# Performance work log

Hardware: AMD Instinct MI355X
Metric: run time of the kernel (lower is better)

## Reference

```python
import jax, jax.numpy as jnp
from jax import lax
import numpy as np

B, DIM, H, W = 4, 256, 64, 64
C2 = 2 * DIM          # 512 internal channels
CB = DIM              # 256 channels per branch
NH = 8                # heads per branch (num_heads*2 // 2)
HD = CB // NH         # 32 head dim
SPLIT = 8
SCALE = HD ** -0.5
EPS = 1e-5


def layernorm(x, g, b):
    mu = jnp.mean(x, axis=-1, keepdims=True)
    var = jnp.mean(jnp.square(x - mu), axis=-1, keepdims=True)
    return (x - mu) * lax.rsqrt(var + EPS) * g + b


def lepe_branch(q, k, v, cw, cb, H_sp, W_sp):
    # q,k,v: [B, L, CB]; cross-shaped stripe-window attention with LePE
    nH, nW = H // H_sp, W // W_sp
    win = H_sp * W_sp

    def to_win(t):
        t = t.reshape(B, nH, H_sp, nW, W_sp, CB).transpose(0, 1, 3, 2, 4, 5)
        return t.reshape(B * nH * nW, win, NH, HD).transpose(0, 2, 1, 3)

    qw = to_win(q) * SCALE
    kw = to_win(k)
    # v as per-window images for depthwise LePE conv: [B*nH*nW, CB, H_sp, W_sp]
    v_img = v.reshape(B, nH, H_sp, nW, W_sp, CB).transpose(0, 1, 3, 5, 2, 4)
    v_img = v_img.reshape(B * nH * nW, CB, H_sp, W_sp)
    lepe = lax.conv_general_dilated(v_img, cw, (1, 1), 'SAME',
                                    feature_group_count=CB,
                                    dimension_numbers=('NCHW', 'OIHW', 'NCHW'))
    lepe = lepe + cb[None, :, None, None]
    vw = v_img.reshape(-1, NH, HD, win).transpose(0, 1, 3, 2)
    lepew = lepe.reshape(-1, NH, HD, win).transpose(0, 1, 3, 2)

    attn = jax.nn.softmax(jnp.einsum('bhid,bhjd->bhij', qw, kw), axis=-1)
    o = jnp.einsum('bhij,bhjd->bhid', attn, vw) + lepew
    # windows back to image token order: [B, H*W, CB]
    o = o.transpose(0, 2, 1, 3).reshape(B, nH, nW, H_sp, W_sp, CB)
    o = o.transpose(0, 1, 3, 2, 4, 5).reshape(B, H * W, CB)
    return o


def setup_inputs() -> dict:
    key = jax.random.key(0)
    ks = jax.random.split(key, 12)
    s = 0.02
    return {
        'x': jax.random.normal(ks[0], (B, DIM, H, W), jnp.float32),
        'w_embed': jax.random.normal(ks[1], (DIM, C2), jnp.float32) * s,
        'g1': 1.0 + jax.random.normal(ks[2], (C2,), jnp.float32) * s,
        'b1': jax.random.normal(ks[3], (C2,), jnp.float32) * s,
        'w_qkv': jax.random.normal(ks[4], (C2, 3 * C2), jnp.float32) * s,
        'conv_w0': jax.random.normal(ks[5], (CB, 1, 3, 3), jnp.float32) * s,
        'conv_b0': jax.random.normal(ks[6], (CB,), jnp.float32) * s,
        'conv_w1': jax.random.normal(ks[7], (CB, 1, 3, 3), jnp.float32) * s,
        'conv_b1': jax.random.normal(ks[8], (CB,), jnp.float32) * s,
        'w_proj': jax.random.normal(ks[9], (C2, C2), jnp.float32) * s,
        'b_proj': jax.random.normal(ks[10], (C2,), jnp.float32) * s,
        'w_out': jax.random.normal(ks[11], (C2, DIM), jnp.float32) * s,
    }


def reference(x, w_embed, g1, b1, w_qkv, conv_w0, conv_b0, conv_w1, conv_b1,
              w_proj, b_proj, w_out):
    L = H * W
    # b c h w -> b (h w) c, then embed to 2*dim
    xt = x.reshape(B, DIM, L).transpose(0, 2, 1)
    x2 = xt @ w_embed                          # [B, L, 512]
    img = layernorm(x2, g1, b1)
    qkv = (img @ w_qkv).reshape(B, L, 3, C2).transpose(2, 0, 1, 3)  # [3,B,L,512]
    q, k, v = qkv[0], qkv[1], qkv[2]
    # branch 0: horizontal stripes (H_sp=H, W_sp=split); branch 1: transpose
    o0 = lepe_branch(q[..., :CB], k[..., :CB], v[..., :CB], conv_w0, conv_b0, H, SPLIT)
    o1 = lepe_branch(q[..., CB:], k[..., CB:], v[..., CB:], conv_w1, conv_b1, SPLIT, W)
    att = jnp.concatenate([o0, o1], axis=2) @ w_proj + b_proj
    xo = x2 + att
    out = (xo @ w_out).transpose(0, 2, 1).reshape(B, DIM, H, W)
    vout = (v @ w_out).transpose(0, 2, 1).reshape(B, DIM, H, W)
    return out, vout
```

## Files before the change

kernel.cpp:

```cpp
#include <hip/hip_runtime.h>
#include <cstdint>

#define Bn 4
#define DIMn 256
#define Ln 4096
#define C2n 512
#define CBn 256
#define HDn 32
#define Mtot (Bn * Ln)

using bf16x8 = __attribute__((ext_vector_type(8))) short;
using f32x4 = __attribute__((ext_vector_type(4))) float;

static constexpr float kScale = 0.17677669529663687f;
static constexpr float kEps = 1e-5f;
static constexpr float kExpC = 0.17677669529663687f * 1.4426950408889634f;

__device__ __forceinline__ ushort f2bf(float f) {
  union {
    float f;
    unsigned u;
  } v;
  v.f = f;
  unsigned r = v.u + 0x7FFFu + ((v.u >> 16) & 1u);
  return (ushort)(r >> 16);
}

__device__ __forceinline__ float bf2f(ushort u) {
  union {
    unsigned u;
    float f;
  } v;
  v.u = (unsigned)u << 16;
  return v.f;
}

__device__ __forceinline__ unsigned cvtpk(float lo, float hi) {
  unsigned r;
  asm("v_cvt_pk_bf16_f32 %0, %1, %2" : "=v"(r) : "v"(lo), "v"(hi));
  return r;
}

__device__ __forceinline__ void gload16(const void* g, void* l) {
  __builtin_amdgcn_global_load_lds(
      (const __attribute__((address_space(1))) unsigned*)g,
      (__attribute__((address_space(3))) unsigned*)l, 16, 0, 0);
}

enum { G_EMBED = 0, G_QKV = 1, G_PROJ = 2, G_OUTT = 3 };

template <int MODE, int ND, int KD, int LDB>
__global__ __launch_bounds__(256) void gemm_bf(
    const ushort* __restrict__ A, const ushort* __restrict__ Bt,
    float* __restrict__ C, const ushort* __restrict__ resid,
    const float* __restrict__ bias, ushort* __restrict__ aux,
    size_t outBase) {
  constexpr int NT = ND / 128;
  __shared__ ushort As[128 * 64];
  __shared__ ushort Bs[128 * 64];

  const int tid = threadIdx.x;
  const int wid = tid >> 6;
  const int lane = tid & 63;
  const int m0 = (blockIdx.x / NT) * 128;
  const int n0 = (blockIdx.x % NT) * 128;

  const int gs = (wid < 2) ? KD : LDB;
  const ushort* gsrc = (wid < 2)
                           ? A + (size_t)(m0 + (wid & 1) * 64) * KD
                           : Bt + (size_t)(n0 + (wid & 1) * 64) * LDB;
  ushort* lbase = (wid < 2 ? As : Bs) + (wid & 1) * (64 * 64);
  const int r8 = lane >> 3;
  const int c8 = lane & 7;

  f32x4 acc[4][4];
#pragma unroll
  for (int i = 0; i < 4; ++i)
#pragma unroll
    for (int j = 0; j < 4; ++j) acc[i][j] = (f32x4){0.f, 0.f, 0.f, 0.f};

  const int wm = (wid & 1) * 64;
  const int wn = (wid >> 1) * 64;
  const int lr = lane & 15;
  const int kq = lane >> 4;

  for (int k0 = 0; k0 < KD; k0 += 64) {
    __syncthreads();
#pragma unroll
    for (int i = 0; i < 8; ++i) {
      const ushort* g = gsrc + (size_t)(i * 8 + r8) * gs + (k0 + c8 * 8);
      gload16(g, lbase + i * 512);
    }
    __syncthreads();
#pragma unroll
    for (int kk = 0; kk < 2; ++kk) {
      bf16x8 af[4], bfr[4];
#pragma unroll
      for (int i = 0; i < 4; ++i)
        af[i] = *(const bf16x8*)(As + (wm + i * 16 + lr) * 64 +
                                 (kk * 4 + kq) * 8);
#pragma unroll
      for (int j = 0; j < 4; ++j)
        bfr[j] = *(const bf16x8*)(Bs + (wn + j * 16 + lr) * 64 +
                                  (kk * 4 + kq) * 8);
#pragma unroll
      for (int i = 0; i < 4; ++i)
#pragma unroll
        for (int j = 0; j < 4; ++j)
          acc[i][j] = __builtin_amdgcn_mfma_f32_16x16x32_bf16(
              af[i], bfr[j], acc[i][j], 0, 0, 0);
    }
  }

#pragma unroll
  for (int i = 0; i < 4; ++i) {
#pragma unroll
    for (int j = 0; j < 4; ++j) {
#pragma unroll
      for (int t = 0; t < 4; ++t) {
        const int mr = m0 + wm + i * 16 + kq * 4 + t;
        const int nc = n0 + wn + j * 16 + lr;
        float val = acc[i][j][t];
        if constexpr (MODE == G_EMBED) {
          aux[(size_t)mr * 512 + nc] = f2bf(val);
        } else if constexpr (MODE == G_QKV) {
          if (nc < 512) val *= kExpC;
          aux[(size_t)mr * 1536 + nc] = f2bf(val);
        } else if constexpr (MODE == G_PROJ) {
          const float v2 =
              val + bf2f(resid[(size_t)mr * 512 + nc]) + bias[nc];
          aux[(size_t)mr * 512 + nc] = f2bf(v2);
        } else {
          C[outBase + ((size_t)(nc >> 12)) * ((size_t)DIMn * Ln) +
            (size_t)mr * Ln + (nc & 4095)] = val;
        }
      }
    }
  }
}

__global__ __launch_bounds__(256) void cvt_w(const float* __restrict__ in,
                                             ushort* __restrict__ out,
                                             int lgK, int N) {
  const int t = blockIdx.x * 256 + threadIdx.x;
  const int K = 1 << lgK;
  const int n = t >> lgK;
  const int k = t & (K - 1);
  out[t] = f2bf(in[(size_t)k * N + n]);
}

__global__ __launch_bounds__(256) void cvt_x(const float* __restrict__ x,
                                             ushort* __restrict__ xe) {
  __shared__ ushort tile[64][65];
  const int blk = blockIdx.x;
  const int lt = blk & 63;
  const int ct = (blk >> 6) & 3;
  const int b = blk >> 8;
  const int l0 = lt * 64, c0 = ct * 64;
  const int t = threadIdx.x;
  const int lanel = t & 63;
  const int grp = t >> 6;
#pragma unroll
  for (int it = 0; it < 16; ++it) {
    const int c = grp * 16 + it;
    tile[c][lanel] =
        f2bf(x[(size_t)b * (DIMn * Ln) + (size_t)(c0 + c) * Ln + l0 + lanel]);
  }
  __syncthreads();
#pragma unroll
  for (int it = 0; it < 16; ++it) {
    const int l = grp * 16 + it;
    xe[((size_t)b * Ln + l0 + l) * 256 + c0 + lanel] = tile[lanel][l];
  }
}

__global__ __launch_bounds__(128) void ln_fuse(const ushort* __restrict__ x2,
                                               const float* __restrict__ g1,
                                               const float* __restrict__ b1,
                                               ushort* __restrict__ xln) {
  const int row = blockIdx.x;
  const int t = threadIdx.x;
  const ushort4 u4 = *(const ushort4*)&x2[(size_t)row * 512 + t * 4];
  float v[4] = {bf2f(u4.x), bf2f(u4.y), bf2f(u4.z), bf2f(u4.w)};
  float s = v[0] + v[1] + v[2] + v[3];
  float s2 = v[0] * v[0] + v[1] * v[1] + v[2] * v[2] + v[3] * v[3];
#pragma unroll
  for (int off = 32; off > 0; off >>= 1) {
    s += __shfl_down(s, off);
    s2 += __shfl_down(s2, off);
  }
  __shared__ float red[4];
  if ((t & 63) == 0) {
    red[t >> 6] = s;
    red[2 + (t >> 6)] = s2;
  }
  __syncthreads();
  const float S = red[0] + red[1];
  const float S2 = red[2] + red[3];
  const float mu = S * (1.f / 512.f);
  const float rs = rsqrtf(S2 * (1.f / 512.f) - mu * mu + kEps);
  const float4 g = *(const float4*)&g1[t * 4];
  const float4 bb = *(const float4*)&b1[t * 4];
  ushort4 o;
  o.x = f2bf((v[0] - mu) * rs * g.x + bb.x);
  o.y = f2bf((v[1] - mu) * rs * g.y + bb.y);
  o.z = f2bf((v[2] - mu) * rs * g.z + bb.z);
  o.w = f2bf((v[3] - mu) * rs * g.w + bb.w);
  *(ushort4*)&xln[(size_t)row * 512 + t * 4] = o;
}

__global__ __launch_bounds__(256, 4) void attn_m(
    const ushort* __restrict__ qkv, ushort* __restrict__ obf,
    const float* __restrict__ cw0, const float* __restrict__ cb0,
    const float* __restrict__ cw1, const float* __restrict__ cb1) {
  __shared__ ushort VtS[32 * 520];
  __shared__ ushort KsS[32 * 40];
  __shared__ float denS[4 * 64];
  __shared__ float cwS[288];
  __shared__ float cbS[32];

  const int blk = blockIdx.x;
  const int branch = blk >> 9;
  const int b = (blk >> 7) & 3;
  const int win = (blk >> 4) & 7;
  const int head = (blk >> 1) & 7;
  const int qh = blk & 1;
  const int tid = threadIdx.x;
  const int w = tid >> 6;
  const int lane = tid & 63;
  const int lr = lane & 15;
  const int kq = lane >> 4;
  const int qcol = branch * CBn + head * HDn;

  const float* cw = branch ? cw1 : cw0;
  const float* cb = branch ? cb1 : cb0;
  for (int i = tid; i < 288; i += 256) cwS[i] = cw[head * 288 + i];
  if (tid < 32) cbS[tid] = cb[head * 32 + tid];

  auto tok2l = [&](int p) -> int {
    return branch == 0 ? ((p >> 3) * 64 + win * 8 + (p & 7)) : (win * 512 + p);
  };
  const size_t rowbase = (size_t)b * Ln;

#pragma unroll
  for (int rr = 0; rr < 2; ++rr) {
    const int j = tid + rr * 256;
    const ushort* vrow = qkv + (rowbase + tok2l(j)) * 1536 + 1024 + qcol;
#pragma unroll
    for (int g = 0; g < 4; ++g) {
      const bf16x8 u = *(const bf16x8*)(vrow + g * 8);
#pragma unroll
      for (int e = 0; e < 8; ++e)
        VtS[(g * 8 + e) * 520 + j] = (ushort)u[e];
    }
  }

  bf16x8 qf[4];
#pragma unroll
  for (int qt = 0; qt < 4; ++qt) {
    const int p = qh * 256 + w * 64 + qt * 16 + lr;
    qf[qt] =
        *(const bf16x8*)(qkv + (rowbase + tok2l(p)) * 1536 + qcol + kq * 8);
  }

  f32x4 acc[4][2];
#pragma unroll
  for (int qt = 0; qt < 4; ++qt) {
    acc[qt][0] = (f32x4){0.f, 0.f, 0.f, 0.f};
    acc[qt][1] = (f32x4){0.f, 0.f, 0.f, 0.f};
  }
  float den[4] = {};
  const f32x4 zero4 = (f32x4){0.f, 0.f, 0.f, 0.f};

  for (int kt = 0; kt < 16; ++kt) {
    const int k0 = kt * 32;
    __syncthreads();
    {
      const int j = tid >> 3;
      const int d0 = (tid & 7) * 4;
      const int row = ((j >> 2) & 1) * 16 + (j >> 3) * 4 + (j & 3);
      const ushort4 k4 = *(const ushort4*)(qkv +
                                           (rowbase + tok2l(k0 + j)) * 1536 +
                                           512 + qcol + d0);
      *(ushort4*)&KsS[row * 40 + d0] = k4;
    }
    __syncthreads();

    const bf16x8 kf0 = *(const bf16x8*)&KsS[lr * 40 + kq * 8];
    const bf16x8 kf1 = *(const bf16x8*)&KsS[(16 + lr) * 40 + kq * 8];
    const bf16x8 vf0 = *(const bf16x8*)&VtS[lr * 520 + k0 + kq * 8];
    const bf16x8 vf1 = *(const bf16x8*)&VtS[(16 + lr) * 520 + k0 + kq * 8];

#pragma unroll
    for (int qt = 0; qt < 4; ++qt) {
      const f32x4 s0 =
          __builtin_amdgcn_mfma_f32_16x16x32_bf16(kf0, qf[qt], zero4, 0, 0, 0);
      const f32x4 s1 =
          __builtin_amdgcn_mfma_f32_16x16x32_bf16(kf1, qf[qt], zero4, 0, 0, 0);
      float e0[4], e1[4];
#pragma unroll
      for (int t = 0; t < 4; ++t) {
        e0[t] = __builtin_amdgcn_exp2f(s0[t]);
        e1[t] = __builtin_amdgcn_exp2f(s1[t]);
      }
      den[qt] += (e0[0] + e0[1] + e0[2] + e0[3]) +
                 (e1[0] + e1[1] + e1[2] + e1[3]);
      union {
        unsigned u[4];
        bf16x8 v;
      } pa;
      pa.u[0] = cvtpk(e0[0], e0[1]);
      pa.u[1] = cvtpk(e0[2], e0[3]);
      pa.u[2] = cvtpk(e1[0], e1[1]);
      pa.u[3] = cvtpk(e1[2], e1[3]);
      acc[qt][0] = __builtin_amdgcn_mfma_f32_16x16x32_bf16(pa.v, vf0,
                                                           acc[qt][0], 0, 0, 0);
      acc[qt][1] = __builtin_amdgcn_mfma_f32_16x16x32_bf16(pa.v, vf1,
                                                           acc[qt][1], 0, 0, 0);
    }
  }

#pragma unroll
  for (int qt = 0; qt < 4; ++qt) {
    float d = den[qt];
    d += __shfl_xor(d, 16);
    d += __shfl_xor(d, 32);
    if (lane < 16) denS[w * 64 + qt * 16 + lr] = d;
  }
  __syncthreads();

  const int Hs = branch ? 8 : 64;
  const int Ws = branch ? 64 : 8;
#pragma unroll
  for (int qt = 0; qt < 4; ++qt) {
#pragma unroll
    for (int t = 0; t < 4; ++t) {
      const int p = qh * 256 + w * 64 + qt * 16 + kq * 4 + t;
      const int l = tok2l(p);
      const int hl = branch ? (p >> 6) : (p >> 3);
      const int wl = branch ? (p & 63) : (p & 7);
      const float inv = 1.f / denS[w * 64 + qt * 16 + kq * 4 + t];
      ushort* orow = obf + ((size_t)b * Ln + l) * 512 + qcol;
#pragma unroll
      for (int dt = 0; dt < 2; ++dt) {
        const int d = dt * 16 + lr;
        float le = cbS[d];
#pragma unroll
        for (int dh = -1; dh <= 1; ++dh) {
          const int hh = hl + dh;
          if (hh < 0 || hh >= Hs) continue;
#pragma unroll
          for (int dw = -1; dw <= 1; ++dw) {
            const int ww = wl + dw;
            if (ww < 0 || ww >= Ws) continue;
            const int pp = hh * Ws + ww;
            le = fmaf(bf2f(VtS[d * 520 + pp]),
                      cwS[d * 9 + (dh + 1) * 3 + (dw + 1)], le);
          }
        }
        orow[d] = f2bf(fmaf(acc[qt][dt][t], inv, le));
      }
    }
  }
}

extern "C" void kernel_launch(void* const* d_in, const int* in_sizes, int n_in,
                              void* d_out, int out_size, void* d_ws,
                              size_t ws_size, hipStream_t stream) {
  const float* x = (const float*)d_in[0];
  const float* w_embed = (const float*)d_in[1];
  const float* g1 = (const float*)d_in[2];
  const float* b1 = (const float*)d_in[3];
  const float* w_qkv = (const float*)d_in[4];
  const float* cw0 = (const float*)d_in[5];
  const float* cb0 = (const float*)d_in[6];
  const float* cw1 = (const float*)d_in[7];
  const float* cb1 = (const float*)d_in[8];
  const float* w_proj = (const float*)d_in[9];
  const float* b_proj = (const float*)d_in[10];
  const float* w_out = (const float*)d_in[11];
  float* out = (float*)d_out;

  char* p = (char*)d_ws;
  ushort* x2bf = (ushort*)p;
  p += (size_t)Mtot * 512 * 2;
  ushort* qkvbf = (ushort*)p;
  p += (size_t)Mtot * 1536 * 2;
  ushort* xe = (ushort*)p;
  ushort* obf = (ushort*)p;
  p += (size_t)Mtot * 512 * 2;
  ushort* xln = (ushort*)p;
  ushort* xobf = (ushort*)p;
  p += (size_t)Mtot * 512 * 2;
  ushort* we_t = (ushort*)p;
  p += (size_t)512 * 256 * 2;
  ushort* wq_t = (ushort*)p;
  p += (size_t)1536 * 512 * 2;
  ushort* wp_t = (ushort*)p;
  p += (size_t)512 * 512 * 2;
  ushort* wo_t = (ushort*)p;

  cvt_w<<<dim3(512 * 256 / 256), 256, 0, stream>>>(w_embed, we_t, 8, 512);
  cvt_w<<<dim3(1536 * 512 / 256), 256, 0, stream>>>(w_qkv, wq_t, 9, 1536);
  cvt_w<<<dim3(512 * 512 / 256), 256, 0, stream>>>(w_proj, wp_t, 9, 512);
  cvt_w<<<dim3(256 * 512 / 256), 256, 0, stream>>>(w_out, wo_t, 9, 256);
  cvt_x<<<dim3(1024), 256, 0, stream>>>(x, xe);

  gemm_bf<G_EMBED, 512, 256, 256><<<dim3(128 * 4), 256, 0, stream>>>(
      xe, we_t, nullptr, nullptr, nullptr, x2bf, 0);
  ln_fuse<<<dim3(Mtot), 128, 0, stream>>>(x2bf, g1, b1, xln);
  gemm_bf<G_QKV, 1536, 512, 512><<<dim3(128 * 12), 256, 0, stream>>>(
      xln, wq_t, nullptr, nullptr, nullptr, qkvbf, 0);
  attn_m<<<dim3(1024), 256, 0, stream>>>(qkvbf, obf, cw0, cb0, cw1, cb1);
  gemm_bf<G_PROJ, 512, 512, 512><<<dim3(128 * 4), 256, 0, stream>>>(
      obf, wp_t, nullptr, x2bf, b_proj, xobf, 0);
  gemm_bf<G_OUTT, Mtot, 512, 512><<<dim3(2 * 128), 256, 0, stream>>>(
      wo_t, xobf, out, nullptr, nullptr, nullptr, 0);
  gemm_bf<G_OUTT, Mtot, 512, 1536><<<dim3(2 * 128), 256, 0, stream>>>(
      wo_t, qkvbf + 1024, out, nullptr, nullptr, nullptr,
      (size_t)Bn * DIMn * Ln);
}
```

Baseline: 192.9 us.

## Merge query halves into 512-thread attention blocks and prefetch K from global into registers

Each attention block now handles all 512 queries of a (branch, batch, window, head) tile with 512 threads instead of two 256-thread blocks. V is transposed into shared memory once per window instead of twice. The per-step K staging through shared memory and its two barriers are removed: each wave loads its K fragments straight from global into registers and prefetches the next step's fragments during the current MFMA work. In exchange, every wave now issues redundant global K loads, there are half as many blocks, and launch bounds no longer promise four blocks per CU, which can change register allocation and occupancy.

```diff
diff --git a/kernel.cpp b/kernel.cpp
--- a/kernel.cpp
+++ b/kernel.cpp
@@ -209,22 +209,20 @@
   *(ushort4*)&xln[(size_t)row * 512 + t * 4] = o;
 }
 
-__global__ __launch_bounds__(256, 4) void attn_m(
+__global__ __launch_bounds__(512) void attn_m(
     const ushort* __restrict__ qkv, ushort* __restrict__ obf,
     const float* __restrict__ cw0, const float* __restrict__ cb0,
     const float* __restrict__ cw1, const float* __restrict__ cb1) {
   __shared__ ushort VtS[32 * 520];
-  __shared__ ushort KsS[32 * 40];
-  __shared__ float denS[4 * 64];
+  __shared__ float denS[8 * 64];
   __shared__ float cwS[288];
   __shared__ float cbS[32];
 
   const int blk = blockIdx.x;
-  const int branch = blk >> 9;
-  const int b = (blk >> 7) & 3;
-  const int win = (blk >> 4) & 7;
-  const int head = (blk >> 1) & 7;
-  const int qh = blk & 1;
+  const int branch = blk >> 8;
+  const int b = (blk >> 6) & 3;
+  const int win = (blk >> 3) & 7;
+  const int head = blk & 7;
   const int tid = threadIdx.x;
   const int w = tid >> 6;
   const int lane = tid & 63;
@@ -234,34 +232,38 @@
 
   const float* cw = branch ? cw1 : cw0;
   const float* cb = branch ? cb1 : cb0;
-  for (int i = tid; i < 288; i += 256) cwS[i] = cw[head * 288 + i];
-  if (tid < 32) cbS[tid] = cb[head * 32 + tid];
+  if (tid < 288) cwS[tid] = cw[head * 288 + tid];
+  if (tid >= 480) cbS[tid - 480] = cb[head * 32 + (tid - 480)];
 
   auto tok2l = [&](int p) -> int {
     return branch == 0 ? ((p >> 3) * 64 + win * 8 + (p & 7)) : (win * 512 + p);
   };
   const size_t rowbase = (size_t)b * Ln;
 
-#pragma unroll
-  for (int rr = 0; rr < 2; ++rr) {
-    const int j = tid + rr * 256;
-    const ushort* vrow = qkv + (rowbase + tok2l(j)) * 1536 + 1024 + qcol;
+  {
+    const ushort* vrow = qkv + (rowbase + tok2l(tid)) * 1536 + 1024 + qcol;
 #pragma unroll
     for (int g = 0; g < 4; ++g) {
       const bf16x8 u = *(const bf16x8*)(vrow + g * 8);
 #pragma unroll
       for (int e = 0; e < 8; ++e)
-        VtS[(g * 8 + e) * 520 + j] = (ushort)u[e];
+        VtS[(g * 8 + e) * 520 + tid] = (ushort)u[e];
     }
   }
 
   bf16x8 qf[4];
 #pragma unroll
   for (int qt = 0; qt < 4; ++qt) {
-    const int p = qh * 256 + w * 64 + qt * 16 + lr;
+    const int p = w * 64 + qt * 16 + lr;
     qf[qt] =
         *(const bf16x8*)(qkv + (rowbase + tok2l(p)) * 1536 + qcol + kq * 8);
   }
+
+  const int j0 = ((lr >> 2) << 3) | (lr & 3);
+  const int j1 = j0 | 4;
+  auto kaddr = [&](int k0, int j) -> const ushort* {
+    return qkv + (rowbase + tok2l(k0 + j)) * 1536 + 512 + qcol + kq * 8;
+  };
 
   f32x4 acc[4][2];
 #pragma unroll
@@ -272,22 +274,19 @@
   float den[4] = {};
   const f32x4 zero4 = (f32x4){0.f, 0.f, 0.f, 0.f};
 
+  bf16x8 kf0 = *(const bf16x8*)kaddr(0, j0);
+  bf16x8 kf1 = *(const bf16x8*)kaddr(0, j1);
+
+  __syncthreads();
+
+#pragma unroll 4
   for (int kt = 0; kt < 16; ++kt) {
     const int k0 = kt * 32;
-    __syncthreads();
-    {
-      const int j = tid >> 3;
-      const int d0 = (tid & 7) * 4;
-      const int row = ((j >> 2) & 1) * 16 + (j >> 3) * 4 + (j & 3);
-      const ushort4 k4 = *(const ushort4*)(qkv +
-                                           (rowbase + tok2l(k0 + j)) * 1536 +
-                                           512 + qcol + d0);
-      *(ushort4*)&KsS[row * 40 + d0] = k4;
-    }
-    __syncthreads();
-
-    const bf16x8 kf0 = *(const bf16x8*)&KsS[lr * 40 + kq * 8];
-    const bf16x8 kf1 = *(const bf16x8*)&KsS[(16 + lr) * 40 + kq * 8];
+    bf16x8 nk0, nk1;
+    if (kt < 15) {
+      nk0 = *(const bf16x8*)kaddr(k0 + 32, j0);
+      nk1 = *(const bf16x8*)kaddr(k0 + 32, j1);
+    }
     const bf16x8 vf0 = *(const bf16x8*)&VtS[lr * 520 + k0 + kq * 8];
     const bf16x8 vf1 = *(const bf16x8*)&VtS[(16 + lr) * 520 + k0 + kq * 8];
 
@@ -318,6 +317,8 @@
       acc[qt][1] = __builtin_amdgcn_mfma_f32_16x16x32_bf16(pa.v, vf1,
                                                            acc[qt][1], 0, 0, 0);
     }
+    kf0 = nk0;
+    kf1 = nk1;
   }
 
 #pragma unroll
@@ -335,7 +336,7 @@
   for (int qt = 0; qt < 4; ++qt) {
 #pragma unroll
     for (int t = 0; t < 4; ++t) {
-      const int p = qh * 256 + w * 64 + qt * 16 + kq * 4 + t;
+      const int p = w * 64 + qt * 16 + kq * 4 + t;
       const int l = tok2l(p);
       const int hl = branch ? (p >> 6) : (p >> 3);
       const int wl = branch ? (p & 63) : (p & 7);
@@ -411,7 +412,7 @@
   ln_fuse<<<dim3(Mtot), 128, 0, stream>>>(x2bf, g1, b1, xln);
   gemm_bf<G_QKV, 1536, 512, 512><<<dim3(128 * 12), 256, 0, stream>>>(
       xln, wq_t, nullptr, nullptr, nullptr, qkvbf, 0);
-  attn_m<<<dim3(1024), 256, 0, stream>>>(qkvbf, obf, cw0, cb0, cw1, cb1);
+  attn_m<<<dim3(512), 512, 0, stream>>>(qkvbf, obf, cw0, cb0, cw1, cb1);
   gemm_bf<G_PROJ, 512, 512, 512><<<dim3(128 * 4), 256, 0, stream>>>(
       obf, wp_t, nullptr, x2bf, b_proj, xobf, 0);
   gemm_bf<G_OUTT, Mtot, 512, 512><<<dim3(2 * 128), 256, 0, stream>>>(
```

Result: slower. 204.2 us (+5.8%).
